# Kernel tuning notes

Hardware: AMD Instinct MI355X
Metric: run time of the kernel (lower is better)

The kernel has to match this reference:

```python
import jax, jax.numpy as jnp
import numpy as np

N, E, D, H, DH, M = 100000, 1600000, 128, 8, 16, 3  # nodes, edges, model_dim, heads, head_dim, views
NEG = -1e9


def setup_inputs() -> dict:
    key = jax.random.key(0)
    ks = jax.random.split(key, 12)
    x = jax.random.normal(ks[0], (N, D), jnp.float32)
    src = jax.random.randint(ks[1], (E,), 0, N)
    dst = jax.random.randint(ks[2], (E,), 0, N)
    pi = jax.random.uniform(ks[3], (N, H, M), jnp.float32)
    pi = pi / pi.sum(-1, keepdims=True)  # router mixture over views
    view_w = jax.random.uniform(ks[4], (E, M), jnp.float32)
    s = 1.0 / np.sqrt(D)
    Wq = jax.random.normal(ks[5], (D, D), jnp.float32) * s
    Wk = jax.random.normal(ks[6], (D, D), jnp.float32) * s
    Wv = jax.random.normal(ks[7], (D, D), jnp.float32) * s
    bq = jax.random.normal(ks[8], (D,), jnp.float32) * 0.02
    bk = jax.random.normal(ks[9], (D,), jnp.float32) * 0.02
    bv = jax.random.normal(ks[10], (D,), jnp.float32) * 0.02
    return {"x": x, "pi": pi, "view_w": view_w, "Wq": Wq, "bq": bq,
            "Wk": Wk, "bk": bk, "Wv": Wv, "bv": bv, "src": src, "dst": dst}


def reference(x, pi, view_w, Wq, bq, Wk, bk, Wv, bv, src, dst):
    n = x.shape[0]
    q = (x @ Wq + bq).reshape(n, H, DH)
    k = (x @ Wk + bk).reshape(n, H, DH)
    v = (x @ Wv + bv).reshape(n, H, DH)
    # per-edge mixture weight: sum over views of pi[dst] * view_w  -> [E, H]
    mix = jnp.einsum('ehm,em->eh', pi[dst], view_w)
    raw = jnp.einsum('ehd,ehd->eh', q[dst], k[src]) / jnp.sqrt(jnp.float32(DH))
    scores = raw + jnp.log(jnp.clip(mix, 1e-8))  # adjacency_mode == 'bias'
    valid = mix > 0
    masked = jnp.where(valid, scores, NEG)
    # scatter-softmax over incoming edges per (node, head)
    smax = jax.ops.segment_max(masked, dst, num_segments=n)
    expv = jnp.where(valid, jnp.exp(masked - smax[dst]), 0.0)
    ssum = jax.ops.segment_sum(expv, dst, num_segments=n)
    attn = expv / jnp.maximum(ssum[dst], 1e-8)  # [E, H]
    # weighted scatter-sum aggregation -> [N, H, DH]
    node_states = jax.ops.segment_sum(v[src] * attn[:, :, None], dst, num_segments=n)
    return node_states, attn
```

## Files before the change

kernel.cpp:

```cpp
#include <hip/hip_runtime.h>
#include <hip/hip_bf16.h>
#include <math.h>

#define SCAN_CHUNK 2048

typedef _Float16 half2v __attribute__((ext_vector_type(2)));
typedef _Float16 half4v __attribute__((ext_vector_type(4)));
typedef _Float16 half8 __attribute__((ext_vector_type(8)));
typedef float floatx4 __attribute__((ext_vector_type(4)));

#if defined(__has_builtin)
#if __has_builtin(__builtin_amdgcn_fdot2)
#define USE_FDOT2 1
#endif
#endif


__global__ void hist_kernel(const int* __restrict__ dst, int* __restrict__ counts, int e) {
    int i = blockIdx.x * blockDim.x + threadIdx.x;
    if (i < e) atomicAdd(&counts[dst[i]], 1);
}

__global__ __launch_bounds__(256) void scan_block_sums(const int* __restrict__ counts,
                                                       int* __restrict__ bsum, int n) {
    __shared__ int sd[256];
    int t = threadIdx.x;
    int base = blockIdx.x * SCAN_CHUNK + t * 8;
    int s = 0;
#pragma unroll
    for (int j = 0; j < 8; ++j) {
        int idx = base + j;
        if (idx < n) s += counts[idx];
    }
    sd[t] = s;
    __syncthreads();
    for (int off = 128; off > 0; off >>= 1) {
        if (t < off) sd[t] += sd[t + off];
        __syncthreads();
    }
    if (t == 0) bsum[blockIdx.x] = sd[0];
}

__global__ void scan_wave(int* bsum, int nb) {
    int lane = threadIdx.x;
    int orig = (lane < nb) ? bsum[lane] : 0;
    int v = orig;
    for (int off = 1; off < 64; off <<= 1) {
        int t = __shfl_up(v, off, 64);
        if (lane >= off) v += t;
    }
    if (lane < nb) bsum[lane] = v - orig;
}

__global__ __launch_bounds__(256) void scan_write(const int* __restrict__ counts,
                                                  const int* __restrict__ bsum,
                                                  int* __restrict__ row_ptr,
                                                  int* __restrict__ cursor,
                                                  int n, int total) {
    __shared__ int sd[256];
    int t = threadIdx.x;
    int base = blockIdx.x * SCAN_CHUNK + t * 8;
    int v[8];
    int s = 0;
#pragma unroll
    for (int j = 0; j < 8; ++j) {
        int idx = base + j;
        v[j] = (idx < n) ? counts[idx] : 0;
        s += v[j];
    }
    sd[t] = s;
    __syncthreads();
    for (int off = 1; off < 256; off <<= 1) {
        int tmp = 0;
        if (t >= off) tmp = sd[t - off];
        __syncthreads();
        if (t >= off) sd[t] += tmp;
        __syncthreads();
    }
    int run = bsum[blockIdx.x] + sd[t] - s;
#pragma unroll
    for (int j = 0; j < 8; ++j) {
        int idx = base + j;
        if (idx < n) {
            row_ptr[idx] = run;
            cursor[idx] = run;
            run += v[j];
        }
    }
    if (blockIdx.x == 0 && t == 0) row_ptr[n] = total;
}

__global__ void fill_csr(const int* __restrict__ dst, const int* __restrict__ src,
                         const float* __restrict__ vw, int* cursor,
                         int4* __restrict__ recs, int* __restrict__ pos, int e) {
    int i = blockIdx.x * blockDim.x + threadIdx.x;
    if (i < e) {
        int p = atomicAdd(&cursor[dst[i]], 1);
        float w0 = vw[3 * i], w1 = vw[3 * i + 1], w2 = vw[3 * i + 2];
        unsigned u0 = (unsigned)__builtin_bit_cast(unsigned short, (_Float16)w0);
        unsigned u1 = (unsigned)__builtin_bit_cast(unsigned short, (_Float16)w1);
        unsigned u2 = (unsigned)__builtin_bit_cast(unsigned short, (_Float16)w2);
        int4 r;
        r.x = src[i];
        r.y = (int)u2;
        r.z = (int)(u0 | (u1 << 16));
        r.w = 0;
        recs[p] = r;
        pos[i] = p;
    }
}


__global__ __launch_bounds__(256) void convert_x(const float* __restrict__ x,
                                                 _Float16* __restrict__ xh, int total8) {
    int i = blockIdx.x * blockDim.x + threadIdx.x;
    if (i < total8) {
        const float4* s = (const float4*)x + i * 2;
        float4 a = s[0], b = s[1];
        half8 h;
        h[0] = (_Float16)a.x; h[1] = (_Float16)a.y; h[2] = (_Float16)a.z; h[3] = (_Float16)a.w;
        h[4] = (_Float16)b.x; h[5] = (_Float16)b.y; h[6] = (_Float16)b.z; h[7] = (_Float16)b.w;
        *((half8*)xh + i) = h;
    }
}

__global__ __launch_bounds__(256) void prep_w(const float* __restrict__ Wq,
                                              const float* __restrict__ Wk,
                                              const float* __restrict__ Wv,
                                              _Float16* __restrict__ wt) {
    const float* W = (blockIdx.x == 0) ? Wq : (blockIdx.x == 1) ? Wk : Wv;
    _Float16* out = wt + (size_t)blockIdx.x * 16384;
    int t = threadIdx.x;
    for (int r = 0; r < 64; ++r) {
        int idx = r * 256 + t;
        int k = idx >> 7, nn = idx & 127;
        out[nn * 128 + k] = (_Float16)W[idx];
    }
}


#define LDP 136

__global__ __launch_bounds__(256) void qkv_mfma(
    const _Float16* __restrict__ xh, const _Float16* __restrict__ wt,
    const float* __restrict__ bq, const float* __restrict__ bk,
    const float* __restrict__ bv,
    _Float16* __restrict__ qh, _Float16* __restrict__ kvb, int n) {
    __shared__ __align__(16) _Float16 xs[128 * LDP];
    __shared__ __align__(16) _Float16 ws[128 * LDP];

    int t = threadIdx.x;
    int tile0 = blockIdx.x * 128;
    int sel = blockIdx.y;
    const _Float16* wsel = wt + (size_t)sel * 16384;
    const float* bias = (sel == 0) ? bq : (sel == 1) ? bk : bv;

#pragma unroll
    for (int r = 0; r < 8; ++r) {
        int id = r * 256 + t;
        int row = id >> 4, c8 = id & 15;
        int grow = tile0 + row;
        half8 val = (half8)(_Float16)0;
        if (grow < n) val = *((const half8*)(xh + (size_t)grow * 128) + c8);
        *((half8*)(xs + row * LDP) + c8) = val;
        half8 wv = *((const half8*)(wsel + row * 128) + c8);
        *((half8*)(ws + row * LDP) + c8) = wv;
    }
    __syncthreads();

    int wave = t >> 6, lane = t & 63;
    int wm = (wave & 1) * 64, wn = (wave >> 1) * 64;
    int lrow = lane & 15, quad = lane >> 4;

    floatx4 acc[4][4];
#pragma unroll
    for (int i = 0; i < 4; ++i)
#pragma unroll
        for (int j = 0; j < 4; ++j) acc[i][j] = (floatx4)0.f;

#pragma unroll
    for (int kk = 0; kk < 4; ++kk) {
        int kbase = kk * 32 + quad * 8;
        half8 a[4], b[4];
#pragma unroll
        for (int i = 0; i < 4; ++i)
            a[i] = *(const half8*)(xs + (wm + i * 16 + lrow) * LDP + kbase);
#pragma unroll
        for (int j = 0; j < 4; ++j)
            b[j] = *(const half8*)(ws + (wn + j * 16 + lrow) * LDP + kbase);
#pragma unroll
        for (int i = 0; i < 4; ++i)
#pragma unroll
            for (int j = 0; j < 4; ++j)
                acc[i][j] = __builtin_amdgcn_mfma_f32_16x16x32_f16(a[i], b[j], acc[i][j], 0, 0, 0);
    }

#pragma unroll
    for (int i = 0; i < 4; ++i) {
#pragma unroll
        for (int j = 0; j < 4; ++j) {
            int col = wn + j * 16 + lrow;
            float bv_ = bias[col];
            int h = col >> 4, dh = col & 15;
            int sub = dh >> 2, w = dh & 3;
#pragma unroll
            for (int r = 0; r < 4; ++r) {
                int row = wm + i * 16 + quad * 4 + r;
                int grow = tile0 + row;
                if (grow < n) {
                    _Float16 val = (_Float16)(acc[i][j][r] + bv_);
                    if (sel == 0)
                        qh[(size_t)grow * 128 + col] = val;
                    else
                        kvb[(size_t)grow * 256 + h * 32 + sub * 8 +
                            (sel == 2 ? 4 : 0) + w] = val;
                }
            }
        }
    }
}


#define STAGE_META(S, idx)                                                    \
    {                                                                         \
        s##S = 0; m##S = 0.f;                                                 \
        if ((idx) < end) {                                                    \
            int4 r_ = recs[(idx)];                                            \
            s##S = r_.x;                                                      \
            half2v w01_ = __builtin_bit_cast(half2v, r_.z);                   \
            _Float16 w2_ =                                                    \
                __builtin_bit_cast(_Float16, (unsigned short)(unsigned)r_.y); \
            m##S = fmaf(p0, (float)w01_[0],                                   \
                        fmaf(p1, (float)w01_[1], p2 * (float)w2_));           \
        }                                                                     \
    }

#define ISSUE_KV(S, idx)                                                      \
    {                                                                         \
        k##S = (half4v)(_Float16)0; v##S = (half4v)(_Float16)0;               \
        if ((idx) < end) {                                                    \
            const _Float16* kp_ = kvbase + (size_t)s##S * 256;                \
            k##S = *(const half4v*)(kp_);                                     \
            v##S = *(const half4v*)(kp_ + 4);                                 \
        }                                                                     \
    }

#ifdef USE_FDOT2
#define DOT4(dres, kS)                                                        \
    {                                                                         \
        half2v x_, y_;                                                        \
        x_[0] = qv[0]; x_[1] = qv[1]; y_[0] = kS[0]; y_[1] = kS[1];           \
        dres = __builtin_amdgcn_fdot2(x_, y_, dres, false);                   \
        x_[0] = qv[2]; x_[1] = qv[3]; y_[0] = kS[2]; y_[1] = kS[3];           \
        dres = __builtin_amdgcn_fdot2(x_, y_, dres, false);                   \
    }
#else
#define DOT4(dres, kS)                                                        \
    {                                                                         \
        _Pragma("unroll")                                                     \
        for (int jj_ = 0; jj_ < 4; ++jj_)                                     \
            dres = fmaf((float)qv[jj_], (float)kS[jj_], dres);                \
    }
#endif

#define COMPUTE(S, mx, slot, validc)                                          \
    {                                                                         \
        float d_ = 0.f;                                                       \
        DOT4(d_, k##S);                                                       \
        d_ += __shfl_xor(d_, 1, 64);                                          \
        d_ += __shfl_xor(d_, 2, 64);                                          \
        float p_ = ((mx) > 0.f) ? (mx)*__expf(d_ * 0.25f) : 0.f;              \
        if (sub == 0 && (validc)) pbuf[(size_t)(slot)*8 + h] = (_Float16)p_;  \
        l += p_;                                                              \
        a0 = fmaf(p_, (float)v##S[0], a0);                                    \
        a1 = fmaf(p_, (float)v##S[1], a1);                                    \
        a2 = fmaf(p_, (float)v##S[2], a2);                                    \
        a3 = fmaf(p_, (float)v##S[3], a3);                                    \
    }

#define BODY(S0, S1, SI0, SI1, jj)                                            \
    {                                                                         \
        ISSUE_KV(SI0, (jj) + 4);                                              \
        ISSUE_KV(SI1, (jj) + 5);                                              \
        float mx0_ = m##S0, mx1_ = m##S1;                                     \
        STAGE_META(S0, (jj) + 6);                                             \
        STAGE_META(S1, (jj) + 7);                                             \
        COMPUTE(S0, mx0_, (jj), true);                                        \
        COMPUTE(S1, mx1_, (jj) + 1, (jj) + 1 < end);                          \
    }

__global__ __launch_bounds__(128, 6) void edge_attn(
    const _Float16* __restrict__ qh, const _Float16* __restrict__ kvb,
    const float* __restrict__ pi,
    const int* __restrict__ row_ptr, const int4* __restrict__ recs,
    float* __restrict__ node_out, float* __restrict__ invb,
    _Float16* __restrict__ pbuf, int n) {
    int t = threadIdx.x;
    int node = blockIdx.x * 4 + (t >> 5);
    if (node >= n) return;
    int q32 = t & 31;
    int h = q32 >> 2, sub = q32 & 3;
    int off = h * 16 + sub * 4;

    const half4v qv = *(const half4v*)(qh + (size_t)node * 128 + off);
    const _Float16* kvbase = kvb + h * 32 + sub * 8;

    float p0 = pi[node * 24 + h * 3 + 0];
    float p1 = pi[node * 24 + h * 3 + 1];
    float p2 = pi[node * 24 + h * 3 + 2];
    int beg = row_ptr[node], end = row_ptr[node + 1];

    float l = 0.f;
    float a0 = 0.f, a1 = 0.f, a2 = 0.f, a3 = 0.f;

    int sA, sB, sC, sD, sE, sF;
    float mA, mB, mC, mD, mE, mF;
    half4v kA, vA, kB, vB, kC, vC, kD, vD, kE, vE, kF, vF;

    STAGE_META(A, beg);
    STAGE_META(B, beg + 1);
    STAGE_META(C, beg + 2);
    STAGE_META(D, beg + 3);
    STAGE_META(E, beg + 4);
    STAGE_META(F, beg + 5);
    ISSUE_KV(A, beg);
    ISSUE_KV(B, beg + 1);
    ISSUE_KV(C, beg + 2);
    ISSUE_KV(D, beg + 3);

    for (int j = beg; j < end;) {
        BODY(A, B, E, F, j);
        j += 2;
        if (j >= end) break;
        BODY(C, D, A, B, j);
        j += 2;
        if (j >= end) break;
        BODY(E, F, C, D, j);
        j += 2;
    }

    float inv = 1.f / fmaxf(l, 1e-8f);
    if (sub == 0) invb[(size_t)node * 8 + h] = inv;

    float4* op = (float4*)(node_out + (size_t)node * 128 + off);
    op[0] = make_float4(a0 * inv, a1 * inv, a2 * inv, a3 * inv);
}


__global__ __launch_bounds__(256) void attn_norm(
    const _Float16* __restrict__ pbuf, const int* __restrict__ dst,
    const int* __restrict__ pos, const float* __restrict__ invb,
    float* __restrict__ attn_out, int e) {
    int i = blockIdx.x * blockDim.x + threadIdx.x;
    if (i < e) {
        int d = dst[i];
        int p = pos[i];
        half8 pv = *((const half8*)pbuf + p);
        const float4* iv = (const float4*)(invb + (size_t)d * 8);
        float4 i0 = iv[0], i1 = iv[1];
        float4* op = (float4*)(attn_out + (size_t)i * 8);
        op[0] = make_float4((float)pv[0] * i0.x, (float)pv[1] * i0.y,
                            (float)pv[2] * i0.z, (float)pv[3] * i0.w);
        op[1] = make_float4((float)pv[4] * i1.x, (float)pv[5] * i1.y,
                            (float)pv[6] * i1.z, (float)pv[7] * i1.w);
    }
}


extern "C" void kernel_launch(void* const* d_in, const int* in_sizes, int n_in,
                              void* d_out, int out_size, void* d_ws, size_t ws_size,
                              hipStream_t stream) {
    const float* x  = (const float*)d_in[0];
    const float* pi = (const float*)d_in[1];
    const float* vw = (const float*)d_in[2];
    const float* Wq = (const float*)d_in[3];
    const float* bq = (const float*)d_in[4];
    const float* Wk = (const float*)d_in[5];
    const float* bk = (const float*)d_in[6];
    const float* Wv = (const float*)d_in[7];
    const float* bv = (const float*)d_in[8];
    const int* src  = (const int*)d_in[9];
    const int* dst  = (const int*)d_in[10];

    int n = in_sizes[0] / 128;
    int e = in_sizes[9];

    _Float16* xh  = (_Float16*)d_ws;
    _Float16* qh  = xh + (size_t)n * 128;
    _Float16* kvb = qh + (size_t)n * 128;
    _Float16* wt  = kvb + (size_t)n * 256;
    _Float16* pbuf = wt + 3 * 16384;
    float* invb  = (float*)(pbuf + (size_t)e * 8);
    int* counts  = (int*)(invb + (size_t)n * 8);
    int* cursor  = counts + n;
    int* row_ptr = cursor + n;
    int* bsum    = row_ptr + n + 1;
    int* pos     = bsum + 64;

    float* node_out = (float*)d_out;
    float* attn_out = node_out + (size_t)n * 128;
    int4* recs = (int4*)attn_out;

    hipMemsetAsync(counts, 0, (size_t)n * sizeof(int), stream);

    int eb = (e + 255) / 256;
    hist_kernel<<<eb, 256, 0, stream>>>(dst, counts, e);

    int nb = (n + SCAN_CHUNK - 1) / SCAN_CHUNK;
    scan_block_sums<<<nb, 256, 0, stream>>>(counts, bsum, n);
    scan_wave<<<1, 64, 0, stream>>>(bsum, nb);
    scan_write<<<nb, 256, 0, stream>>>(counts, bsum, row_ptr, cursor, n, e);
    fill_csr<<<eb, 256, 0, stream>>>(dst, src, vw, cursor, recs, pos, e);

    int tot8 = (n * 128) / 8;
    convert_x<<<(tot8 + 255) / 256, 256, 0, stream>>>(x, xh, tot8);
    prep_w<<<3, 256, 0, stream>>>(Wq, Wk, Wv, wt);

    int gtiles = (n + 127) / 128;
    qkv_mfma<<<dim3(gtiles, 3), 256, 0, stream>>>(xh, wt, bq, bk, bv, qh, kvb, n);

    int gb = (n + 3) / 4;
    edge_attn<<<gb, 128, 0, stream>>>(qh, kvb, pi, row_ptr, recs,
                                      node_out, invb, pbuf, n);
    attn_norm<<<eb, 256, 0, stream>>>(pbuf, dst, pos, invb, attn_out, e);
}
```

Before: 611.9 us.

## Fuse x conversion into QKV GEMM and replace scan with atomic row allocation

Drops the separate convert_x pass; the QKV MFMA kernel now loads fp32 x and converts to fp16 while staging into shared memory. The three-kernel prefix scan becomes a single kernel that takes a wave-level scan and reserves each wave's edge range with a global atomic. CSR rows are therefore no longer in node order, and edge_attn computes the row end from counts. Weight prep and zeroing of counts are merged into one setup kernel that replaces the memset. The aim is fewer launches and less memory traffic, at the cost of reading fp32 x three times (once per Q/K/V block) and a less node-ordered edge layout.

After: 622.6 us. About the same (+1.7%).

```diff
diff --git a/kernel.cpp b/kernel.cpp
--- a/kernel.cpp
+++ b/kernel.cpp
@@ -1,8 +1,6 @@
 #include <hip/hip_runtime.h>
 #include <hip/hip_bf16.h>
 #include <math.h>
-
-#define SCAN_CHUNK 2048
 
 typedef _Float16 half2v __attribute__((ext_vector_type(2)));
 typedef _Float16 half4v __attribute__((ext_vector_type(4)));
@@ -16,78 +14,58 @@
 #endif
 
 
+__global__ __launch_bounds__(256) void setup(
+    const float* __restrict__ Wq, const float* __restrict__ Wk,
+    const float* __restrict__ Wv, _Float16* __restrict__ wt,
+    int* __restrict__ counts, int* __restrict__ gcur, int n) {
+    int b = blockIdx.x;
+    int t = threadIdx.x;
+    if (b < 3) {
+        const float* W = (b == 0) ? Wq : (b == 1) ? Wk : Wv;
+        _Float16* out = wt + (size_t)b * 16384;
+        for (int r = 0; r < 64; ++r) {
+            int idx = r * 256 + t;
+            int k = idx >> 7, nn = idx & 127;
+            out[nn * 128 + k] = (_Float16)W[idx];
+        }
+    } else {
+        if (b == 3 && t == 0) *gcur = 0;
+        int base = (b - 3) * 1024 + t * 4;
+#pragma unroll
+        for (int j = 0; j < 4; ++j) {
+            int idx = base + j;
+            if (idx < n) counts[idx] = 0;
+        }
+    }
+}
+
+
 __global__ void hist_kernel(const int* __restrict__ dst, int* __restrict__ counts, int e) {
     int i = blockIdx.x * blockDim.x + threadIdx.x;
     if (i < e) atomicAdd(&counts[dst[i]], 1);
 }
 
-__global__ __launch_bounds__(256) void scan_block_sums(const int* __restrict__ counts,
-                                                       int* __restrict__ bsum, int n) {
-    __shared__ int sd[256];
-    int t = threadIdx.x;
-    int base = blockIdx.x * SCAN_CHUNK + t * 8;
-    int s = 0;
-#pragma unroll
-    for (int j = 0; j < 8; ++j) {
-        int idx = base + j;
-        if (idx < n) s += counts[idx];
-    }
-    sd[t] = s;
-    __syncthreads();
-    for (int off = 128; off > 0; off >>= 1) {
-        if (t < off) sd[t] += sd[t + off];
-        __syncthreads();
-    }
-    if (t == 0) bsum[blockIdx.x] = sd[0];
-}
-
-__global__ void scan_wave(int* bsum, int nb) {
-    int lane = threadIdx.x;
-    int orig = (lane < nb) ? bsum[lane] : 0;
-    int v = orig;
+
+__global__ __launch_bounds__(256) void row_alloc(
+    const int* __restrict__ counts, int* __restrict__ row_ptr,
+    int* __restrict__ cursor, int* __restrict__ gcur, int n) {
+    int i = blockIdx.x * blockDim.x + threadIdx.x;
+    int lane = threadIdx.x & 63;
+    int deg = (i < n) ? counts[i] : 0;
+    int incl = deg;
     for (int off = 1; off < 64; off <<= 1) {
-        int t = __shfl_up(v, off, 64);
-        if (lane >= off) v += t;
-    }
-    if (lane < nb) bsum[lane] = v - orig;
-}
-
-__global__ __launch_bounds__(256) void scan_write(const int* __restrict__ counts,
-                                                  const int* __restrict__ bsum,
-                                                  int* __restrict__ row_ptr,
-                                                  int* __restrict__ cursor,
-                                                  int n, int total) {
-    __shared__ int sd[256];
-    int t = threadIdx.x;
-    int base = blockIdx.x * SCAN_CHUNK + t * 8;
-    int v[8];
-    int s = 0;
-#pragma unroll
-    for (int j = 0; j < 8; ++j) {
-        int idx = base + j;
-        v[j] = (idx < n) ? counts[idx] : 0;
-        s += v[j];
-    }
-    sd[t] = s;
-    __syncthreads();
-    for (int off = 1; off < 256; off <<= 1) {
-        int tmp = 0;
-        if (t >= off) tmp = sd[t - off];
-        __syncthreads();
-        if (t >= off) sd[t] += tmp;
-        __syncthreads();
-    }
-    int run = bsum[blockIdx.x] + sd[t] - s;
-#pragma unroll
-    for (int j = 0; j < 8; ++j) {
-        int idx = base + j;
-        if (idx < n) {
-            row_ptr[idx] = run;
-            cursor[idx] = run;
-            run += v[j];
-        }
-    }
-    if (blockIdx.x == 0 && t == 0) row_ptr[n] = total;
+        int tmp = __shfl_up(incl, off, 64);
+        if (lane >= off) incl += tmp;
+    }
+    int wave_total = __shfl(incl, 63, 64);
+    int base = 0;
+    if (lane == 63) base = atomicAdd(gcur, wave_total);
+    base = __shfl(base, 63, 64);
+    int beg = base + incl - deg;
+    if (i < n) {
+        row_ptr[i] = beg;
+        cursor[i] = beg;
+    }
 }
 
 __global__ void fill_csr(const int* __restrict__ dst, const int* __restrict__ src,
@@ -111,38 +89,10 @@
 }
 
 
-__global__ __launch_bounds__(256) void convert_x(const float* __restrict__ x,
-                                                 _Float16* __restrict__ xh, int total8) {
-    int i = blockIdx.x * blockDim.x + threadIdx.x;
-    if (i < total8) {
-        const float4* s = (const float4*)x + i * 2;
-        float4 a = s[0], b = s[1];
-        half8 h;
-        h[0] = (_Float16)a.x; h[1] = (_Float16)a.y; h[2] = (_Float16)a.z; h[3] = (_Float16)a.w;
-        h[4] = (_Float16)b.x; h[5] = (_Float16)b.y; h[6] = (_Float16)b.z; h[7] = (_Float16)b.w;
-        *((half8*)xh + i) = h;
-    }
-}
-
-__global__ __launch_bounds__(256) void prep_w(const float* __restrict__ Wq,
-                                              const float* __restrict__ Wk,
-                                              const float* __restrict__ Wv,
-                                              _Float16* __restrict__ wt) {
-    const float* W = (blockIdx.x == 0) ? Wq : (blockIdx.x == 1) ? Wk : Wv;
-    _Float16* out = wt + (size_t)blockIdx.x * 16384;
-    int t = threadIdx.x;
-    for (int r = 0; r < 64; ++r) {
-        int idx = r * 256 + t;
-        int k = idx >> 7, nn = idx & 127;
-        out[nn * 128 + k] = (_Float16)W[idx];
-    }
-}
-
-
 #define LDP 136
 
 __global__ __launch_bounds__(256) void qkv_mfma(
-    const _Float16* __restrict__ xh, const _Float16* __restrict__ wt,
+    const float* __restrict__ x, const _Float16* __restrict__ wt,
     const float* __restrict__ bq, const float* __restrict__ bk,
     const float* __restrict__ bv,
     _Float16* __restrict__ qh, _Float16* __restrict__ kvb, int n) {
@@ -161,7 +111,14 @@
         int row = id >> 4, c8 = id & 15;
         int grow = tile0 + row;
         half8 val = (half8)(_Float16)0;
-        if (grow < n) val = *((const half8*)(xh + (size_t)grow * 128) + c8);
+        if (grow < n) {
+            const float4* s = (const float4*)(x + (size_t)grow * 128 + c8 * 8);
+            float4 a = s[0], b = s[1];
+            val[0] = (_Float16)a.x; val[1] = (_Float16)a.y;
+            val[2] = (_Float16)a.z; val[3] = (_Float16)a.w;
+            val[4] = (_Float16)b.x; val[5] = (_Float16)b.y;
+            val[6] = (_Float16)b.z; val[7] = (_Float16)b.w;
+        }
         *((half8*)(xs + row * LDP) + c8) = val;
         half8 wv = *((const half8*)(wsel + row * 128) + c8);
         *((half8*)(ws + row * LDP) + c8) = wv;
@@ -292,7 +249,8 @@
 __global__ __launch_bounds__(128, 6) void edge_attn(
     const _Float16* __restrict__ qh, const _Float16* __restrict__ kvb,
     const float* __restrict__ pi,
-    const int* __restrict__ row_ptr, const int4* __restrict__ recs,
+    const int* __restrict__ row_ptr, const int* __restrict__ counts,
+    const int4* __restrict__ recs,
     float* __restrict__ node_out, float* __restrict__ invb,
     _Float16* __restrict__ pbuf, int n) {
     int t = threadIdx.x;
@@ -308,7 +266,8 @@
     float p0 = pi[node * 24 + h * 3 + 0];
     float p1 = pi[node * 24 + h * 3 + 1];
     float p2 = pi[node * 24 + h * 3 + 2];
-    int beg = row_ptr[node], end = row_ptr[node + 1];
+    int beg = row_ptr[node];
+    int end = beg + counts[node];
 
     float l = 0.f;
     float a0 = 0.f, a1 = 0.f, a2 = 0.f, a3 = 0.f;
@@ -385,8 +344,7 @@
     int n = in_sizes[0] / 128;
     int e = in_sizes[9];
 
-    _Float16* xh  = (_Float16*)d_ws;
-    _Float16* qh  = xh + (size_t)n * 128;
+    _Float16* qh  = (_Float16*)d_ws;
     _Float16* kvb = qh + (size_t)n * 128;
     _Float16* wt  = kvb + (size_t)n * 256;
     _Float16* pbuf = wt + 3 * 16384;
@@ -394,33 +352,28 @@
     int* counts  = (int*)(invb + (size_t)n * 8);
     int* cursor  = counts + n;
     int* row_ptr = cursor + n;
-    int* bsum    = row_ptr + n + 1;
-    int* pos     = bsum + 64;
+    int* pos     = row_ptr + n + 1;
+    int* gcur    = pos + e;
 
     float* node_out = (float*)d_out;
     float* attn_out = node_out + (size_t)n * 128;
     int4* recs = (int4*)attn_out;
 
-    hipMemsetAsync(counts, 0, (size_t)n * sizeof(int), stream);
+    int zb = (n + 1023) / 1024;
+    setup<<<3 + zb, 256, 0, stream>>>(Wq, Wk, Wv, wt, counts, gcur, n);
 
     int eb = (e + 255) / 256;
     hist_kernel<<<eb, 256, 0, stream>>>(dst, counts, e);
 
-    int nb = (n + SCAN_CHUNK - 1) / SCAN_CHUNK;
-    scan_block_sums<<<nb, 256, 0, stream>>>(counts, bsum, n);
-    scan_wave<<<1, 64, 0, stream>>>(bsum, nb);
-    scan_write<<<nb, 256, 0, stream>>>(counts, bsum, row_ptr, cursor, n, e);
+    int nblk = (n + 255) / 256;
+    row_alloc<<<nblk, 256, 0, stream>>>(counts, row_ptr, cursor, gcur, n);
     fill_csr<<<eb, 256, 0, stream>>>(dst, src, vw, cursor, recs, pos, e);
 
-    int tot8 = (n * 128) / 8;
-    convert_x<<<(tot8 + 255) / 256, 256, 0, stream>>>(x, xh, tot8);
-    prep_w<<<3, 256, 0, stream>>>(Wq, Wk, Wv, wt);
-
     int gtiles = (n + 127) / 128;
-    qkv_mfma<<<dim3(gtiles, 3), 256, 0, stream>>>(xh, wt, bq, bk, bv, qh, kvb, n);
+    qkv_mfma<<<dim3(gtiles, 3), 256, 0, stream>>>(x, wt, bq, bk, bv, qh, kvb, n);
 
     int gb = (n + 3) / 4;
-    edge_attn<<<gb, 128, 0, stream>>>(qh, kvb, pi, row_ptr, recs,
+    edge_attn<<<gb, 128, 0, stream>>>(qh, kvb, pi, row_ptr, counts, recs,
                                       node_out, invb, pbuf, n);
     attn_norm<<<eb, 256, 0, stream>>>(pbuf, dst, pos, invb, attn_out, e);
 }
```
